# Kernel optimization log

Hardware: AMD Instinct MI355X
Metric: run time of the kernel (lower is better)

The kernel has to match this reference:

```python
import jax, jax.numpy as jnp
import numpy as np

INPUT_DIM, HIDDEN, CB_DIM, CB_SIZE = 768, 512, 256, 512
COMMIT_W = 1.0


def setup_inputs() -> dict:
    key = jax.random.key(0)
    ks = jax.random.split(key, 10)
    def lin(k, fan_in, fan_out):
        lim = 1.0 / np.sqrt(fan_in)
        return jax.random.uniform(k, (fan_in, fan_out), jnp.float32, -lim, lim)
    return {
        "x": jax.random.normal(ks[0], (32, 2048, INPUT_DIM), jnp.float32),
        "W1": lin(ks[1], INPUT_DIM, HIDDEN),
        "b1": jnp.zeros((HIDDEN,), jnp.float32),
        "W2": lin(ks[2], HIDDEN, CB_DIM),
        "b2": jnp.zeros((CB_DIM,), jnp.float32),
        "codebook": jax.random.normal(ks[3], (CB_SIZE, CB_DIM), jnp.float32),
        "W3": lin(ks[4], CB_DIM, HIDDEN),
        "b3": jnp.zeros((HIDDEN,), jnp.float32),
        "W4": lin(ks[5], HIDDEN, INPUT_DIM),
        "b4": jnp.zeros((INPUT_DIM,), jnp.float32),
    }


def reference(x, W1, b1, W2, b2, codebook, W3, b3, W4, b4):
    # encoder MLP: [b, n, 768] -> [b, n, 256]
    h = jax.nn.relu(jnp.einsum('bnd,dh->bnh', x, W1) + b1)
    z = jnp.einsum('bnh,hc->bnc', h, W2) + b2

    # VQ: squared-L2 distance to codebook, argmin, gather
    # d(z, c) = ||z||^2 - 2 z.c + ||c||^2  (||z||^2 constant over argmin, omitted)
    dots = jnp.einsum('bnc,kc->bnk', z, codebook)          # [b, n, K]
    c_sq = jnp.sum(codebook * codebook, axis=-1)            # [K]
    indices = jnp.argmin(c_sq - 2.0 * dots, axis=-1)        # [b, n] int
    q = codebook[indices]                                   # [b, n, 256] gather

    # straight-through estimator + commitment loss
    quantized = z + jax.lax.stop_gradient(q - z)
    commit_loss = COMMIT_W * jnp.mean((z - jax.lax.stop_gradient(q)) ** 2)

    # decoder MLP: [b, n, 256] -> [b, n, 768]
    h2 = jax.nn.relu(jnp.einsum('bnc,ch->bnh', quantized, W3) + b3)
    recon = jnp.einsum('bnh,hd->bnd', h2, W4) + b4
    return recon, indices.astype(jnp.int32), commit_loss
```

## Files before the change

### kernel.cpp

```cpp
#include <hip/hip_runtime.h>

typedef unsigned short u16;
typedef unsigned int   u32;
typedef __attribute__((ext_vector_type(8))) short short8;
typedef __attribute__((ext_vector_type(4))) float f32x4;

#define NTOK 65536
#define IND  768
#define HID  512
#define CBD  256
#define CBS  512

#define OUT_IDX_OFF   ((size_t)NTOK * IND)
#define OUT_LOSS_OFF  (OUT_IDX_OFF + NTOK)

#define OFF_H      ((size_t)0)
#define OFF_Z      ((size_t)134217728)
#define OFF_W1H    ((size_t)201326592)
#define OFF_W1L    ((size_t)202113024)
#define OFF_W2H    ((size_t)202899456)
#define OFF_W2L    ((size_t)203161600)
#define OFF_CBH    ((size_t)203423744)
#define OFF_CBL    ((size_t)203685888)
#define OFF_CSQ    ((size_t)203948032)
#define OFF_PART   ((size_t)0)
#define OFF_TABLE  ((size_t)8388608)
#define OFF_ZSQ    ((size_t)9961472)
#define OFF_IDX    ((size_t)10223616)
#define OFF_FLAGS  ((size_t)10485760)
#define OFF_CNT    ((size_t)10747904)

__device__ __forceinline__ u16 f2bf(float f) {
    u32 u = __float_as_uint(f);
    return (u16)((u + 0x7fffu + ((u >> 16) & 1u)) >> 16);
}
__device__ __forceinline__ float bf2f(u16 h) {
    return __uint_as_float(((u32)h) << 16);
}

__global__ __launch_bounds__(256) void cbsplit(
    const float* __restrict__ cb, u16* __restrict__ hi, u16* __restrict__ lo,
    float* __restrict__ csq)
{
    int c = blockIdx.x, t = threadIdx.x;
    float v = cb[(size_t)c * CBD + t];
    u16 h = f2bf(v); u16 l = f2bf(v - bf2f(h));
    hi[(size_t)c * CBD + t] = h; lo[(size_t)c * CBD + t] = l;
    __shared__ float red[256];
    red[t] = v * v; __syncthreads();
    for (int s = 128; s; s >>= 1) { if (t < s) red[t] += red[t + s]; __syncthreads(); }
    if (!t) csq[c] = red[0];
}

__global__ __launch_bounds__(256) void wsplit(
    const float* __restrict__ W, u16* __restrict__ hi, u16* __restrict__ lo,
    int K, int N)
{
    int n = blockIdx.x;
    for (int k = threadIdx.x; k < K; k += 256) {
        float v = W[(size_t)k * N + n];
        u16 h = f2bf(v); u16 l = f2bf(v - bf2f(h));
        hi[(size_t)n * K + k] = h; lo[(size_t)n * K + k] = l;
    }
}

#define CHS 1040
#define PLN (4 * CHS)

template<int AMODE, int EPI>
__global__ __launch_bounds__(256, 2) void gemm3(
    const float* __restrict__ Af, const u32* __restrict__ Apk,
    const u16* __restrict__ Bhi, const u16* __restrict__ Blo,
    const float* __restrict__ bias,
    u32* __restrict__ Opk, float* __restrict__ Opart,
    int M, int N, int K)
{
    __shared__ u16 lds[4 * PLN];
    u16* sAh = lds;
    u16* sAl = lds + PLN;
    u16* sBh = lds + 2 * PLN;
    u16* sBl = lds + 3 * PLN;
    const int tid  = threadIdx.x;

    const int nwg = gridDim.x * gridDim.y;
    const int hw  = blockIdx.y * gridDim.x + blockIdx.x;
    const int logical = (hw & 7) * (nwg >> 3) + (hw >> 3);
    const int bx = logical % gridDim.x;
    const int by = logical / gridDim.x;

    const int m0 = by * 128, n0 = bx * 128;
    const int w = tid >> 6, lane = tid & 63, quad = lane >> 4, l15 = lane & 15;
    const int wm = (w & 1) * 64, wn = (w >> 1) * 64;

    f32x4 acc[4][4] = {};

    for (int k0 = 0; k0 < K; k0 += 32) {
        __syncthreads();
        if (AMODE == 0) {
            #pragma unroll
            for (int s = 0; s < 4; ++s) {
                int slot = tid + s * 256;
                int m = slot >> 3, kg = (slot & 7) << 2;
                int c = kg >> 3, off = kg & 7;
                float4 v = *(const float4*)(Af + (size_t)(m0 + m) * K + k0 + kg);
                u16 h0 = f2bf(v.x), h1 = f2bf(v.y), h2 = f2bf(v.z), h3 = f2bf(v.w);
                ushort4 hv = {h0, h1, h2, h3};
                ushort4 lv = {f2bf(v.x - bf2f(h0)), f2bf(v.y - bf2f(h1)),
                              f2bf(v.z - bf2f(h2)), f2bf(v.w - bf2f(h3))};
                *(ushort4*)&sAh[c * CHS + m * 8 + off] = hv;
                *(ushort4*)&sAl[c * CHS + m * 8 + off] = lv;
            }
        } else {
            #pragma unroll
            for (int s = 0; s < 4; ++s) {
                int slot = tid + s * 256;
                int m = slot >> 3, ke = (slot & 7) << 2;
                int c = ke >> 3, off = ke & 7;
                uint4 u = *(const uint4*)(Apk + (size_t)(m0 + m) * K + k0 + ke);
                ushort4 hv = {(u16)(u.x & 0xffff), (u16)(u.y & 0xffff),
                              (u16)(u.z & 0xffff), (u16)(u.w & 0xffff)};
                ushort4 lv = {(u16)(u.x >> 16), (u16)(u.y >> 16),
                              (u16)(u.z >> 16), (u16)(u.w >> 16)};
                *(ushort4*)&sAh[c * CHS + m * 8 + off] = hv;
                *(ushort4*)&sAl[c * CHS + m * 8 + off] = lv;
            }
        }
        #pragma unroll
        for (int s = 0; s < 4; ++s) {
            int slot = tid + s * 256;
            int n = (slot & 511) >> 2, ku = slot & 3;
            const u16* src = (slot < 512) ? Bhi : Blo;
            u16* dst = (slot < 512) ? sBh : sBl;
            uint4 u = *(const uint4*)(src + (size_t)(n0 + n) * K + k0 + ku * 8);
            *(uint4*)&dst[ku * CHS + n * 8] = u;
        }
        __syncthreads();

        short8 ah[4], al[4], bh[4], bl[4];
        const int kc = quad * CHS;
        #pragma unroll
        for (int i = 0; i < 4; ++i) {
            int ar = wm + i * 16 + l15;
            int br = wn + i * 16 + l15;
            ah[i] = *(const short8*)&sAh[kc + ar * 8];
            al[i] = *(const short8*)&sAl[kc + ar * 8];
            bh[i] = *(const short8*)&sBh[kc + br * 8];
            bl[i] = *(const short8*)&sBl[kc + br * 8];
        }
        #pragma unroll
        for (int i = 0; i < 4; ++i)
            #pragma unroll
            for (int j = 0; j < 4; ++j) {
                acc[i][j] = __builtin_amdgcn_mfma_f32_16x16x32_bf16(ah[i], bh[j], acc[i][j], 0, 0, 0);
                acc[i][j] = __builtin_amdgcn_mfma_f32_16x16x32_bf16(ah[i], bl[j], acc[i][j], 0, 0, 0);
                acc[i][j] = __builtin_amdgcn_mfma_f32_16x16x32_bf16(al[i], bh[j], acc[i][j], 0, 0, 0);
            }
    }

    if (EPI <= 1) {
        float bn[4];
        #pragma unroll
        for (int j = 0; j < 4; ++j) bn[j] = bias[n0 + wn + j * 16 + l15];
        #pragma unroll
        for (int i = 0; i < 4; ++i)
            #pragma unroll
            for (int r = 0; r < 4; ++r) {
                int row = m0 + wm + i * 16 + quad * 4 + r;
                #pragma unroll
                for (int j = 0; j < 4; ++j) {
                    float v = acc[i][j][r] + bn[j];
                    if (EPI == 0) v = fmaxf(v, 0.f);
                    u16 h = f2bf(v); u16 l = f2bf(v - bf2f(h));
                    Opk[(size_t)row * N + n0 + wn + j * 16 + l15] = (u32)h | ((u32)l << 16);
                }
            }
    } else {
        float cs[4]; int cidx[4];
        #pragma unroll
        for (int j = 0; j < 4; ++j) {
            cidx[j] = n0 + wn + j * 16 + l15;
            cs[j] = bias[cidx[j]];
        }
        const int nparts = gridDim.x * 2;
        const int pslot  = bx * 2 + (w >> 1);
        #pragma unroll
        for (int i = 0; i < 4; ++i)
            #pragma unroll
            for (int r = 0; r < 4; ++r) {
                int row = m0 + wm + i * 16 + quad * 4 + r;
                float d1 = 3.4e38f, d2 = 3.4e38f; int i1 = 0x7fffffff;
                #pragma unroll
                for (int j = 0; j < 4; ++j) {
                    float v = fmaf(-2.0f, acc[i][j][r], cs[j]);
                    if (v < d1) { d2 = d1; d1 = v; i1 = cidx[j]; }
                    else d2 = fminf(d2, v);
                }
                #pragma unroll
                for (int mm = 1; mm < 16; mm <<= 1) {
                    float od1 = __shfl_xor(d1, mm, 64);
                    float od2 = __shfl_xor(d2, mm, 64);
                    int   oi1 = __shfl_xor(i1, mm, 64);
                    if (od1 < d1 || (od1 == d1 && oi1 < i1)) { d2 = fminf(d1, od2); d1 = od1; i1 = oi1; }
                    else d2 = fminf(d2, od1);
                }
                if (l15 == 0) {
                    float4 o = {d1, d2, __int_as_float(i1), 0.f};
                    *(float4*)&Opart[((size_t)row * nparts + pslot) * 4] = o;
                }
            }
    }
}

__global__ __launch_bounds__(256) void zsq_pk(
    const u32* __restrict__ Zpk, float* __restrict__ zsq)
{
    int tok = blockIdx.x * 4 + (threadIdx.x >> 6);
    int lane = threadIdx.x & 63;
    uint4 u = *(const uint4*)(Zpk + (size_t)tok * CBD + lane * 4);
    float z0 = bf2f((u16)(u.x & 0xffff)) + bf2f((u16)(u.x >> 16));
    float z1 = bf2f((u16)(u.y & 0xffff)) + bf2f((u16)(u.y >> 16));
    float z2 = bf2f((u16)(u.z & 0xffff)) + bf2f((u16)(u.z >> 16));
    float z3 = bf2f((u16)(u.w & 0xffff)) + bf2f((u16)(u.w >> 16));
    float s = z0 * z0 + z1 * z1 + z2 * z2 + z3 * z3;
    #pragma unroll
    for (int off = 32; off; off >>= 1) s += __shfl_down(s, off, 64);
    if (!lane) zsq[tok] = s;
}

__global__ __launch_bounds__(256) void vq_reduce(
    const float* __restrict__ part, const float* __restrict__ zsq,
    float* __restrict__ out_idx, int* __restrict__ idx_i,
    int* __restrict__ cnt, float* __restrict__ accum, int* __restrict__ flags)
{
    int tok = blockIdx.x * 256 + threadIdx.x;
    float d1 = 3.4e38f, d2 = 3.4e38f; int i1 = 0x7fffffff;
    #pragma unroll
    for (int nb = 0; nb < 8; ++nb) {
        float4 p = *(const float4*)&part[((size_t)tok * 8 + nb) * 4];
        float pd1 = p.x, pd2 = p.y; int pi1 = __float_as_int(p.z);
        if (pd1 < d1 || (pd1 == d1 && pi1 < i1)) { d2 = fminf(d1, pd2); d1 = pd1; i1 = pi1; }
        else d2 = fminf(d2, pd1);
    }
    out_idx[tok] = (float)i1;
    idx_i[tok] = i1;
    if (d2 - d1 < 0.01f) {
        int p = atomicAdd(cnt, 1);
        if (p >= 0 && p < NTOK) flags[p] = tok;
    }
    float c = zsq[tok] + d1;
    __shared__ float red[256];
    red[threadIdx.x] = c; __syncthreads();
    for (int s = 128; s; s >>= 1) { if (threadIdx.x < s) red[threadIdx.x] += red[threadIdx.x + s]; __syncthreads(); }
    if (!threadIdx.x) atomicAdd(accum, red[0]);
}

__device__ __forceinline__ void fma16(float (&a)[4][4],
    float x0, float x1, float x2, float x3, float4 w)
{
    a[0][0] = fmaf(x0, w.x, a[0][0]); a[0][1] = fmaf(x0, w.y, a[0][1]);
    a[0][2] = fmaf(x0, w.z, a[0][2]); a[0][3] = fmaf(x0, w.w, a[0][3]);
    a[1][0] = fmaf(x1, w.x, a[1][0]); a[1][1] = fmaf(x1, w.y, a[1][1]);
    a[1][2] = fmaf(x1, w.z, a[1][2]); a[1][3] = fmaf(x1, w.w, a[1][3]);
    a[2][0] = fmaf(x2, w.x, a[2][0]); a[2][1] = fmaf(x2, w.y, a[2][1]);
    a[2][2] = fmaf(x2, w.z, a[2][2]); a[2][3] = fmaf(x2, w.w, a[2][3]);
    a[3][0] = fmaf(x3, w.x, a[3][0]); a[3][1] = fmaf(x3, w.y, a[3][1]);
    a[3][2] = fmaf(x3, w.z, a[3][2]); a[3][3] = fmaf(x3, w.w, a[3][3]);
}
__device__ __forceinline__ void fma8(float (&a)[2][4],
    float x0, float x1, float4 w)
{
    a[0][0] = fmaf(x0, w.x, a[0][0]); a[0][1] = fmaf(x0, w.y, a[0][1]);
    a[0][2] = fmaf(x0, w.z, a[0][2]); a[0][3] = fmaf(x0, w.w, a[0][3]);
    a[1][0] = fmaf(x1, w.x, a[1][0]); a[1][1] = fmaf(x1, w.y, a[1][1]);
    a[1][2] = fmaf(x1, w.z, a[1][2]); a[1][3] = fmaf(x1, w.w, a[1][3]);
}

__global__ __launch_bounds__(256) void fixup(
    const int* __restrict__ cnt, const int* __restrict__ flags,
    const float* __restrict__ x, const float* __restrict__ W1, const float* __restrict__ b1,
    const float* __restrict__ W2, const float* __restrict__ b2,
    const float* __restrict__ cb, const float* __restrict__ csq,
    int* __restrict__ idx_i, float* __restrict__ out_idx)
{
    __shared__ float xs[8][IND];
    __shared__ float hs[8][HID];
    __shared__ float zs[8][CBD];
    __shared__ float csq_s[CBS];
    __shared__ float bd_s[4][8];
    __shared__ int   bi_s[4][8];
    __shared__ int   tok_s[8];

    int n = cnt[0]; if (n > NTOK) n = NTOK; if (n < 0) n = 0;
    const int t = threadIdx.x;
    const int nb = (n + 7) >> 3;

    if (t < 128) *(float4*)&csq_s[t * 4] = *(const float4*)(csq + t * 4);

    for (int ib = blockIdx.x; ib < nb; ib += gridDim.x) {
        const int base = ib * 8;
        __syncthreads();
        if (t < 8) {
            int fi = base + t; if (fi > n - 1) fi = n - 1;
            tok_s[t] = flags[fi];
        }
        __syncthreads();

        #pragma unroll
        for (int s = 0; s < 6; ++s) {
            int slot = t + s * 256;
            int tt = slot / 192, c4 = slot - tt * 192;
            *(float4*)&xs[tt][c4 * 4] =
                *(const float4*)(x + (size_t)tok_s[tt] * IND + c4 * 4);
        }
        __syncthreads();

        {
            const int tg4 = (t >> 7) * 4;
            const int j0 = (t & 127) * 4;
            float a[4][4];
            float4 bb = *(const float4*)(b1 + j0);
            #pragma unroll
            for (int ti = 0; ti < 4; ++ti) {
                a[ti][0] = bb.x; a[ti][1] = bb.y; a[ti][2] = bb.z; a[ti][3] = bb.w;
            }
            const float* Wb = W1 + j0;
#define LW1(s, K4) { const int _k = (((K4) < 192) ? (K4) : 191) * 2048;        \
            s##0 = *(const float4*)(Wb + _k);                                  \
            s##1 = *(const float4*)(Wb + _k + 512);                            \
            s##2 = *(const float4*)(Wb + _k + 1024);                           \
            s##3 = *(const float4*)(Wb + _k + 1536); }
#define CMP1(s, K4) {                                                          \
            float4 xv0 = *(const float4*)&xs[tg4 + 0][(K4) * 4];               \
            float4 xv1 = *(const float4*)&xs[tg4 + 1][(K4) * 4];               \
            float4 xv2 = *(const float4*)&xs[tg4 + 2][(K4) * 4];               \
            float4 xv3 = *(const float4*)&xs[tg4 + 3][(K4) * 4];               \
            fma16(a, xv0.x, xv1.x, xv2.x, xv3.x, s##0);                        \
            fma16(a, xv0.y, xv1.y, xv2.y, xv3.y, s##1);                        \
            fma16(a, xv0.z, xv1.z, xv2.z, xv3.z, s##2);                        \
            fma16(a, xv0.w, xv1.w, xv2.w, xv3.w, s##3); }
            float4 wA0, wA1, wA2, wA3, wB0, wB1, wB2, wB3;
            float4 wC0, wC1, wC2, wC3, wD0, wD1, wD2, wD3;
            LW1(wA, 0); LW1(wB, 1); LW1(wC, 2);
            for (int k4 = 0; k4 < 192; k4 += 4) {
                LW1(wD, k4 + 3); CMP1(wA, k4 + 0);
                LW1(wA, k4 + 4); CMP1(wB, k4 + 1);
                LW1(wB, k4 + 5); CMP1(wC, k4 + 2);
                LW1(wC, k4 + 6); CMP1(wD, k4 + 3);
            }
#undef LW1
#undef CMP1
            #pragma unroll
            for (int ti = 0; ti < 4; ++ti) {
                float4 o = {fmaxf(a[ti][0], 0.f), fmaxf(a[ti][1], 0.f),
                            fmaxf(a[ti][2], 0.f), fmaxf(a[ti][3], 0.f)};
                *(float4*)&hs[tg4 + ti][j0] = o;
            }
        }
        __syncthreads();

        {
            const int tg2 = (t >> 6) * 2;
            const int c0 = (t & 63) * 4;
            float az[2][4];
            float4 bz = *(const float4*)(b2 + c0);
            #pragma unroll
            for (int ti = 0; ti < 2; ++ti) {
                az[ti][0] = bz.x; az[ti][1] = bz.y; az[ti][2] = bz.z; az[ti][3] = bz.w;
            }
            const float* Wb = W2 + c0;
#define LW2(s, K4) { const int _k = (((K4) < 128) ? (K4) : 127) * 1024;        \
            s##0 = *(const float4*)(Wb + _k);                                  \
            s##1 = *(const float4*)(Wb + _k + 256);                            \
            s##2 = *(const float4*)(Wb + _k + 512);                            \
            s##3 = *(const float4*)(Wb + _k + 768); }
#define CMP2(s, K4) {                                                          \
            float4 hv0 = *(const float4*)&hs[tg2 + 0][(K4) * 4];               \
            float4 hv1 = *(const float4*)&hs[tg2 + 1][(K4) * 4];               \
            fma8(az, hv0.x, hv1.x, s##0);                                      \
            fma8(az, hv0.y, hv1.y, s##1);                                      \
            fma8(az, hv0.z, hv1.z, s##2);                                      \
            fma8(az, hv0.w, hv1.w, s##3); }
            float4 wA0, wA1, wA2, wA3, wB0, wB1, wB2, wB3;
            float4 wC0, wC1, wC2, wC3, wD0, wD1, wD2, wD3;
            LW2(wA, 0); LW2(wB, 1); LW2(wC, 2);
            for (int k4 = 0; k4 < 128; k4 += 4) {
                LW2(wD, k4 + 3); CMP2(wA, k4 + 0);
                LW2(wA, k4 + 4); CMP2(wB, k4 + 1);
                LW2(wB, k4 + 5); CMP2(wC, k4 + 2);
                LW2(wC, k4 + 6); CMP2(wD, k4 + 3);
            }
#undef LW2
#undef CMP2
            #pragma unroll
            for (int ti = 0; ti < 2; ++ti) {
                float4 o = {az[ti][0], az[ti][1], az[ti][2], az[ti][3]};
                *(float4*)&zs[tg2 + ti][c0] = o;
            }
        }
        __syncthreads();

        {
            const int wv = t >> 6, l = t & 63;
            const float* cb0 = cb + (size_t)t * CBD;
            const float* cb1 = cb + (size_t)(t + 256) * CBD;
            float d0[8], d1[8];
            #pragma unroll
            for (int tt = 0; tt < 8; ++tt) { d0[tt] = 0.f; d1[tt] = 0.f; }
            float4 pA = *(const float4*)(cb0);
            float4 pB = *(const float4*)(cb1);
            for (int k4 = 0; k4 < 64; ++k4) {
                float4 cA = pA, cB = pB;
                int kn = (k4 + 1 < 64) ? (k4 + 1) : 63;
                pA = *(const float4*)(cb0 + kn * 4);
                pB = *(const float4*)(cb1 + kn * 4);
                #pragma unroll
                for (int tt = 0; tt < 8; ++tt) {
                    float4 zv = *(const float4*)&zs[tt][k4 * 4];
                    d0[tt] = fmaf(zv.w, cA.w, fmaf(zv.z, cA.z,
                             fmaf(zv.y, cA.y, fmaf(zv.x, cA.x, d0[tt]))));
                    d1[tt] = fmaf(zv.w, cB.w, fmaf(zv.z, cB.z,
                             fmaf(zv.y, cB.y, fmaf(zv.x, cB.x, d1[tt]))));
                }
            }
            float bd[8]; int bi[8];
            const float cs0 = csq_s[t], cs1 = csq_s[t + 256];
            #pragma unroll
            for (int tt = 0; tt < 8; ++tt) {
                float e0 = cs0 - 2.f * d0[tt];
                float e1 = cs1 - 2.f * d1[tt];
                if (e0 <= e1) { bd[tt] = e0; bi[tt] = t; }
                else          { bd[tt] = e1; bi[tt] = t + 256; }
            }
            #pragma unroll
            for (int mm = 1; mm < 64; mm <<= 1) {
                #pragma unroll
                for (int tt = 0; tt < 8; ++tt) {
                    float od = __shfl_xor(bd[tt], mm, 64);
                    int   oi = __shfl_xor(bi[tt], mm, 64);
                    if (od < bd[tt] || (od == bd[tt] && oi < bi[tt])) { bd[tt] = od; bi[tt] = oi; }
                }
            }
            if (l == 0) {
                #pragma unroll
                for (int tt = 0; tt < 8; ++tt) { bd_s[wv][tt] = bd[tt]; bi_s[wv][tt] = bi[tt]; }
            }
        }
        __syncthreads();

        if (t < 8) {
            const int tt = t;
            float d = bd_s[0][tt]; int i = bi_s[0][tt];
            #pragma unroll
            for (int wv = 1; wv < 4; ++wv) {
                float od = bd_s[wv][tt]; int oi = bi_s[wv][tt];
                if (od < d || (od == d && oi < i)) { d = od; i = oi; }
            }
            if (base + tt < n) {
                int tok = tok_s[tt];
                idx_i[tok] = i; out_idx[tok] = (float)i;
            }
        }
        __syncthreads();
    }
}

__global__ __launch_bounds__(256) void table_pre(
    const float* __restrict__ cb, const float* __restrict__ W3,
    const float* __restrict__ b3, const float* __restrict__ W4,
    const float* __restrict__ b4, float* __restrict__ table)
{
    __shared__ float crow[CBD];
    __shared__ float h2[HID];
    const int c = blockIdx.x;
    const int t = threadIdx.x;
    crow[t] = cb[(size_t)c * CBD + t];
    __syncthreads();
    #pragma unroll
    for (int s = 0; s < 2; ++s) {
        int j = t + s * 256;
        float acc = b3[j];
        for (int k = 0; k < CBD; ++k) acc = fmaf(crow[k], W3[(size_t)k * HID + j], acc);
        h2[j] = fmaxf(acc, 0.f);
    }
    __syncthreads();
    #pragma unroll
    for (int s = 0; s < 3; ++s) {
        int j = t + s * 256;
        float acc = b4[j];
        for (int k = 0; k < HID; ++k) acc = fmaf(h2[k], W4[(size_t)k * IND + j], acc);
        table[(size_t)c * IND + j] = acc;
    }
}

__global__ __launch_bounds__(256) void gather_kernel(
    const int* __restrict__ idx, const float* __restrict__ table,
    float* __restrict__ out)
{
    unsigned i = blockIdx.x * 256u + threadIdx.x;
    unsigned tok = i / 192u;
    unsigned c = i - tok * 192u;
    int id = idx[tok];
    ((float4*)out)[i] = ((const float4*)table)[(size_t)id * 192 + c];
}

__global__ void finalize_kernel(const float* __restrict__ accum,
                                float* __restrict__ out_loss)
{
    out_loss[0] = accum[0] * (1.0f / 16777216.0f);
}

extern "C" void kernel_launch(void* const* d_in, const int* in_sizes, int n_in,
                              void* d_out, int out_size, void* d_ws, size_t ws_size,
                              hipStream_t stream) {
    const float* x  = (const float*)d_in[0];
    const float* W1 = (const float*)d_in[1];
    const float* b1 = (const float*)d_in[2];
    const float* W2 = (const float*)d_in[3];
    const float* b2 = (const float*)d_in[4];
    const float* cb = (const float*)d_in[5];
    const float* W3 = (const float*)d_in[6];
    const float* b3 = (const float*)d_in[7];
    const float* W4 = (const float*)d_in[8];
    const float* b4 = (const float*)d_in[9];

    char* ws = (char*)d_ws;
    u32*  Hpk   = (u32*)(ws + OFF_H);
    u32*  Zpk   = (u32*)(ws + OFF_Z);
    u16*  W1h   = (u16*)(ws + OFF_W1H);
    u16*  W1l   = (u16*)(ws + OFF_W1L);
    u16*  W2h   = (u16*)(ws + OFF_W2H);
    u16*  W2l   = (u16*)(ws + OFF_W2L);
    u16*  CBh   = (u16*)(ws + OFF_CBH);
    u16*  CBl   = (u16*)(ws + OFF_CBL);
    float* csq  = (float*)(ws + OFF_CSQ);
    float* part = (float*)(ws + OFF_PART);
    float* table = (float*)(ws + OFF_TABLE);
    float* zsq  = (float*)(ws + OFF_ZSQ);
    int*   idx_i = (int*)(ws + OFF_IDX);
    int*   flags = (int*)(ws + OFF_FLAGS);
    int*   cnt   = (int*)(ws + OFF_CNT);
    float* accum = (float*)(ws + OFF_CNT + 4);

    float* out      = (float*)d_out;
    float* out_idx  = out + OUT_IDX_OFF;
    float* out_loss = out + OUT_LOSS_OFF;

    cbsplit<<<CBS, 256, 0, stream>>>(cb, CBh, CBl, csq);
    wsplit<<<HID, 256, 0, stream>>>(W1, W1h, W1l, IND, HID);
    wsplit<<<CBD, 256, 0, stream>>>(W2, W2h, W2l, HID, CBD);

    gemm3<0, 0><<<dim3(HID / 128, NTOK / 128), 256, 0, stream>>>(
        x, (const u32*)nullptr, W1h, W1l, b1, Hpk, (float*)nullptr, NTOK, HID, IND);
    gemm3<1, 1><<<dim3(CBD / 128, NTOK / 128), 256, 0, stream>>>(
        (const float*)nullptr, Hpk, W2h, W2l, b2, Zpk, (float*)nullptr, NTOK, CBD, HID);

    hipMemsetAsync(cnt, 0, 8, stream);

    zsq_pk<<<NTOK / 4, 256, 0, stream>>>(Zpk, zsq);

    gemm3<1, 2><<<dim3(CBS / 128, NTOK / 128), 256, 0, stream>>>(
        (const float*)nullptr, Zpk, CBh, CBl, csq, (u32*)nullptr, part, NTOK, CBS, CBD);

    table_pre<<<CBS, 256, 0, stream>>>(cb, W3, b3, W4, b4, table);

    vq_reduce<<<NTOK / 256, 256, 0, stream>>>(part, zsq, out_idx, idx_i, cnt, accum, flags);

    fixup<<<1024, 256, 0, stream>>>(cnt, flags, x, W1, b1, W2, b2, cb, csq, idx_i, out_idx);

    gather_kernel<<<(NTOK * (IND / 4)) / 256, 256, 0, stream>>>(idx_i, table, out);

    finalize_kernel<<<1, 1, 0, stream>>>(accum, out_loss);
}
```

Before: 972.9 us.

## Split fp32 VQ fixup into tiled batched GEMM passes over flagged tokens

The single fused fixup kernel, which recomputed encoder and distances for 8 flagged tokens at a time while streaming W1/W2 from global memory, is replaced by three kernels. Two are a 64x64 shared-memory tiled fp32 GEMM, the first gathering flagged rows of x and the second producing z, followed by a distance/argmin kernel that processes 32 tokens per block. Work is done in chunks of up to 32768 flagged tokens, with intermediates staged in workspace. This gives weight reuse across many tokens, at the cost of six extra launches and intermediate global traffic even when few tokens are flagged.

Measured after the change: 875.6 us. 10.0% less time.

```diff
diff --git a/kernel.cpp b/kernel.cpp
--- a/kernel.cpp
+++ b/kernel.cpp
@@ -29,6 +29,9 @@
 #define OFF_IDX    ((size_t)10223616)
 #define OFF_FLAGS  ((size_t)10485760)
 #define OFF_CNT    ((size_t)10747904)
+#define OFF_HFIX   ((size_t)16777216)
+#define OFF_ZFIX   ((size_t)83886080)
+#define FCHUNK 32768
 
 __device__ __forceinline__ u16 f2bf(float f) {
     u32 u = __float_as_uint(f);
@@ -266,141 +269,120 @@
     a[3][0] = fmaf(x3, w.x, a[3][0]); a[3][1] = fmaf(x3, w.y, a[3][1]);
     a[3][2] = fmaf(x3, w.z, a[3][2]); a[3][3] = fmaf(x3, w.w, a[3][3]);
 }
-__device__ __forceinline__ void fma8(float (&a)[2][4],
-    float x0, float x1, float4 w)
-{
-    a[0][0] = fmaf(x0, w.x, a[0][0]); a[0][1] = fmaf(x0, w.y, a[0][1]);
-    a[0][2] = fmaf(x0, w.z, a[0][2]); a[0][3] = fmaf(x0, w.w, a[0][3]);
-    a[1][0] = fmaf(x1, w.x, a[1][0]); a[1][1] = fmaf(x1, w.y, a[1][1]);
-    a[1][2] = fmaf(x1, w.z, a[1][2]); a[1][3] = fmaf(x1, w.w, a[1][3]);
-}
-
-__global__ __launch_bounds__(256) void fixup(
-    const int* __restrict__ cnt, const int* __restrict__ flags,
-    const float* __restrict__ x, const float* __restrict__ W1, const float* __restrict__ b1,
-    const float* __restrict__ W2, const float* __restrict__ b2,
-    const float* __restrict__ cb, const float* __restrict__ csq,
+
+template<int K, int N, int RELU, int MODE>
+__global__ __launch_bounds__(256) void fixup_gemm(
+    const int* __restrict__ cnt, const int* __restrict__ flags, int base,
+    const float* __restrict__ A, const float* __restrict__ W,
+    const float* __restrict__ bias, float* __restrict__ C)
+{
+    __shared__ float xs[64][68];
+    __shared__ float Wt[64][68];
+    __shared__ int   tok_s[64];
+    int n = cnt[0]; if (n > NTOK) n = NTOK;
+    int nc = n - base; if (nc <= 0) return; if (nc > FCHUNK) nc = FCHUNK;
+    const int ntile = (nc + 63) >> 6;
+    const int items = ntile * (N >> 6);
+    const int t = threadIdx.x;
+    const int tg4 = (t >> 4) << 2;
+    const int cg  = t & 15;
+
+    for (int it = blockIdx.x; it < items; it += gridDim.x) {
+        const int tt = it / (N >> 6);
+        const int ct = it - tt * (N >> 6);
+        const int j0 = ct * 64;
+        const int trow = tt * 64;
+        __syncthreads();
+        if (MODE == 0 && t < 64) {
+            int fi = base + trow + t; if (fi > n - 1) fi = n - 1;
+            tok_s[t] = flags[fi];
+        }
+        __syncthreads();
+
+        float a[4][4];
+        float4 bb = *(const float4*)(bias + j0 + cg * 4);
+        #pragma unroll
+        for (int ti = 0; ti < 4; ++ti) {
+            a[ti][0] = bb.x; a[ti][1] = bb.y; a[ti][2] = bb.z; a[ti][3] = bb.w;
+        }
+
+        for (int k0 = 0; k0 < K; k0 += 64) {
+            __syncthreads();
+            #pragma unroll
+            for (int s = 0; s < 4; ++s) {
+                int slot = t + s * 256;
+                int row = slot >> 4, c4 = slot & 15;
+                const float* src = (MODE == 0)
+                    ? A + (size_t)tok_s[row] * K + k0 + c4 * 4
+                    : A + (size_t)(trow + row) * K + k0 + c4 * 4;
+                *(float4*)&xs[row][c4 * 4] = *(const float4*)src;
+            }
+            #pragma unroll
+            for (int s = 0; s < 4; ++s) {
+                int slot = t + s * 256;
+                int kk = slot >> 4, c4 = slot & 15;
+                *(float4*)&Wt[kk][c4 * 4] =
+                    *(const float4*)(W + (size_t)(k0 + kk) * N + j0 + c4 * 4);
+            }
+            __syncthreads();
+            #pragma unroll 4
+            for (int k4 = 0; k4 < 16; ++k4) {
+                float4 xv0 = *(const float4*)&xs[tg4 + 0][k4 * 4];
+                float4 xv1 = *(const float4*)&xs[tg4 + 1][k4 * 4];
+                float4 xv2 = *(const float4*)&xs[tg4 + 2][k4 * 4];
+                float4 xv3 = *(const float4*)&xs[tg4 + 3][k4 * 4];
+                float4 w0 = *(const float4*)&Wt[k4 * 4 + 0][cg * 4];
+                float4 w1 = *(const float4*)&Wt[k4 * 4 + 1][cg * 4];
+                float4 w2 = *(const float4*)&Wt[k4 * 4 + 2][cg * 4];
+                float4 w3 = *(const float4*)&Wt[k4 * 4 + 3][cg * 4];
+                fma16(a, xv0.x, xv1.x, xv2.x, xv3.x, w0);
+                fma16(a, xv0.y, xv1.y, xv2.y, xv3.y, w1);
+                fma16(a, xv0.z, xv1.z, xv2.z, xv3.z, w2);
+                fma16(a, xv0.w, xv1.w, xv2.w, xv3.w, w3);
+            }
+        }
+        #pragma unroll
+        for (int ti = 0; ti < 4; ++ti) {
+            float4 o;
+            if (RELU) {
+                o.x = fmaxf(a[ti][0], 0.f); o.y = fmaxf(a[ti][1], 0.f);
+                o.z = fmaxf(a[ti][2], 0.f); o.w = fmaxf(a[ti][3], 0.f);
+            } else {
+                o.x = a[ti][0]; o.y = a[ti][1]; o.z = a[ti][2]; o.w = a[ti][3];
+            }
+            *(float4*)&C[(size_t)(trow + tg4 + ti) * N + j0 + cg * 4] = o;
+        }
+    }
+}
+
+__global__ __launch_bounds__(256) void fixup_d(
+    const int* __restrict__ cnt, const int* __restrict__ flags, int base,
+    const float* __restrict__ zbuf, const float* __restrict__ cb,
+    const float* __restrict__ csq,
     int* __restrict__ idx_i, float* __restrict__ out_idx)
 {
-    __shared__ float xs[8][IND];
-    __shared__ float hs[8][HID];
-    __shared__ float zs[8][CBD];
+    __shared__ float zs[32][CBD];
     __shared__ float csq_s[CBS];
     __shared__ float bd_s[4][8];
     __shared__ int   bi_s[4][8];
-    __shared__ int   tok_s[8];
-
-    int n = cnt[0]; if (n > NTOK) n = NTOK; if (n < 0) n = 0;
+    int n = cnt[0]; if (n > NTOK) n = NTOK;
+    int nc = n - base; if (nc <= 0) return; if (nc > FCHUNK) nc = FCHUNK;
+    const int ntile = (nc + 31) >> 5;
     const int t = threadIdx.x;
-    const int nb = (n + 7) >> 3;
-
+    const int wv = t >> 6, l = t & 63;
     if (t < 128) *(float4*)&csq_s[t * 4] = *(const float4*)(csq + t * 4);
 
-    for (int ib = blockIdx.x; ib < nb; ib += gridDim.x) {
-        const int base = ib * 8;
+    for (int it = blockIdx.x; it < ntile; it += gridDim.x) {
         __syncthreads();
-        if (t < 8) {
-            int fi = base + t; if (fi > n - 1) fi = n - 1;
-            tok_s[t] = flags[fi];
+        #pragma unroll
+        for (int s = 0; s < 8; ++s) {
+            int slot = t + s * 256;
+            int row = slot >> 6, c4 = slot & 63;
+            *(float4*)&zs[row][c4 * 4] =
+                *(const float4*)(zbuf + (size_t)(it * 32 + row) * CBD + c4 * 4);
         }
         __syncthreads();
-
-        #pragma unroll
-        for (int s = 0; s < 6; ++s) {
-            int slot = t + s * 256;
-            int tt = slot / 192, c4 = slot - tt * 192;
-            *(float4*)&xs[tt][c4 * 4] =
-                *(const float4*)(x + (size_t)tok_s[tt] * IND + c4 * 4);
-        }
-        __syncthreads();
-
-        {
-            const int tg4 = (t >> 7) * 4;
-            const int j0 = (t & 127) * 4;
-            float a[4][4];
-            float4 bb = *(const float4*)(b1 + j0);
-            #pragma unroll
-            for (int ti = 0; ti < 4; ++ti) {
-                a[ti][0] = bb.x; a[ti][1] = bb.y; a[ti][2] = bb.z; a[ti][3] = bb.w;
-            }
-            const float* Wb = W1 + j0;
-#define LW1(s, K4) { const int _k = (((K4) < 192) ? (K4) : 191) * 2048;        \
-            s##0 = *(const float4*)(Wb + _k);                                  \
-            s##1 = *(const float4*)(Wb + _k + 512);                            \
-            s##2 = *(const float4*)(Wb + _k + 1024);                           \
-            s##3 = *(const float4*)(Wb + _k + 1536); }
-#define CMP1(s, K4) {                                                          \
-            float4 xv0 = *(const float4*)&xs[tg4 + 0][(K4) * 4];               \
-            float4 xv1 = *(const float4*)&xs[tg4 + 1][(K4) * 4];               \
-            float4 xv2 = *(const float4*)&xs[tg4 + 2][(K4) * 4];               \
-            float4 xv3 = *(const float4*)&xs[tg4 + 3][(K4) * 4];               \
-            fma16(a, xv0.x, xv1.x, xv2.x, xv3.x, s##0);                        \
-            fma16(a, xv0.y, xv1.y, xv2.y, xv3.y, s##1);                        \
-            fma16(a, xv0.z, xv1.z, xv2.z, xv3.z, s##2);                        \
-            fma16(a, xv0.w, xv1.w, xv2.w, xv3.w, s##3); }
-            float4 wA0, wA1, wA2, wA3, wB0, wB1, wB2, wB3;
-            float4 wC0, wC1, wC2, wC3, wD0, wD1, wD2, wD3;
-            LW1(wA, 0); LW1(wB, 1); LW1(wC, 2);
-            for (int k4 = 0; k4 < 192; k4 += 4) {
-                LW1(wD, k4 + 3); CMP1(wA, k4 + 0);
-                LW1(wA, k4 + 4); CMP1(wB, k4 + 1);
-                LW1(wB, k4 + 5); CMP1(wC, k4 + 2);
-                LW1(wC, k4 + 6); CMP1(wD, k4 + 3);
-            }
-#undef LW1
-#undef CMP1
-            #pragma unroll
-            for (int ti = 0; ti < 4; ++ti) {
-                float4 o = {fmaxf(a[ti][0], 0.f), fmaxf(a[ti][1], 0.f),
-                            fmaxf(a[ti][2], 0.f), fmaxf(a[ti][3], 0.f)};
-                *(float4*)&hs[tg4 + ti][j0] = o;
-            }
-        }
-        __syncthreads();
-
-        {
-            const int tg2 = (t >> 6) * 2;
-            const int c0 = (t & 63) * 4;
-            float az[2][4];
-            float4 bz = *(const float4*)(b2 + c0);
-            #pragma unroll
-            for (int ti = 0; ti < 2; ++ti) {
-                az[ti][0] = bz.x; az[ti][1] = bz.y; az[ti][2] = bz.z; az[ti][3] = bz.w;
-            }
-            const float* Wb = W2 + c0;
-#define LW2(s, K4) { const int _k = (((K4) < 128) ? (K4) : 127) * 1024;        \
-            s##0 = *(const float4*)(Wb + _k);                                  \
-            s##1 = *(const float4*)(Wb + _k + 256);                            \
-            s##2 = *(const float4*)(Wb + _k + 512);                            \
-            s##3 = *(const float4*)(Wb + _k + 768); }
-#define CMP2(s, K4) {                                                          \
-            float4 hv0 = *(const float4*)&hs[tg2 + 0][(K4) * 4];               \
-            float4 hv1 = *(const float4*)&hs[tg2 + 1][(K4) * 4];               \
-            fma8(az, hv0.x, hv1.x, s##0);                                      \
-            fma8(az, hv0.y, hv1.y, s##1);                                      \
-            fma8(az, hv0.z, hv1.z, s##2);                                      \
-            fma8(az, hv0.w, hv1.w, s##3); }
-            float4 wA0, wA1, wA2, wA3, wB0, wB1, wB2, wB3;
-            float4 wC0, wC1, wC2, wC3, wD0, wD1, wD2, wD3;
-            LW2(wA, 0); LW2(wB, 1); LW2(wC, 2);
-            for (int k4 = 0; k4 < 128; k4 += 4) {
-                LW2(wD, k4 + 3); CMP2(wA, k4 + 0);
-                LW2(wA, k4 + 4); CMP2(wB, k4 + 1);
-                LW2(wB, k4 + 5); CMP2(wC, k4 + 2);
-                LW2(wC, k4 + 6); CMP2(wD, k4 + 3);
-            }
-#undef LW2
-#undef CMP2
-            #pragma unroll
-            for (int ti = 0; ti < 2; ++ti) {
-                float4 o = {az[ti][0], az[ti][1], az[ti][2], az[ti][3]};
-                *(float4*)&zs[tg2 + ti][c0] = o;
-            }
-        }
-        __syncthreads();
-
-        {
-            const int wv = t >> 6, l = t & 63;
+        for (int sb = 0; sb < 4; ++sb) {
             const float* cb0 = cb + (size_t)t * CBD;
             const float* cb1 = cb + (size_t)(t + 256) * CBD;
             float d0[8], d1[8];
@@ -415,7 +397,7 @@
                 pB = *(const float4*)(cb1 + kn * 4);
                 #pragma unroll
                 for (int tt = 0; tt < 8; ++tt) {
-                    float4 zv = *(const float4*)&zs[tt][k4 * 4];
+                    float4 zv = *(const float4*)&zs[sb * 8 + tt][k4 * 4];
                     d0[tt] = fmaf(zv.w, cA.w, fmaf(zv.z, cA.z,
                              fmaf(zv.y, cA.y, fmaf(zv.x, cA.x, d0[tt]))));
                     d1[tt] = fmaf(zv.w, cB.w, fmaf(zv.z, cB.z,
@@ -444,23 +426,23 @@
                 #pragma unroll
                 for (int tt = 0; tt < 8; ++tt) { bd_s[wv][tt] = bd[tt]; bi_s[wv][tt] = bi[tt]; }
             }
-        }
-        __syncthreads();
-
-        if (t < 8) {
-            const int tt = t;
-            float d = bd_s[0][tt]; int i = bi_s[0][tt];
-            #pragma unroll
-            for (int wv = 1; wv < 4; ++wv) {
-                float od = bd_s[wv][tt]; int oi = bi_s[wv][tt];
-                if (od < d || (od == d && oi < i)) { d = od; i = oi; }
-            }
-            if (base + tt < n) {
-                int tok = tok_s[tt];
-                idx_i[tok] = i; out_idx[tok] = (float)i;
-            }
-        }
-        __syncthreads();
+            __syncthreads();
+            if (t < 8) {
+                const int tt = t;
+                float d = bd_s[0][tt]; int i = bi_s[0][tt];
+                #pragma unroll
+                for (int v2 = 1; v2 < 4; ++v2) {
+                    float od = bd_s[v2][tt]; int oi = bi_s[v2][tt];
+                    if (od < d || (od == d && oi < i)) { d = od; i = oi; }
+                }
+                int fi = base + it * 32 + sb * 8 + tt;
+                if (fi < n) {
+                    int tok = flags[fi];
+                    idx_i[tok] = i; out_idx[tok] = (float)i;
+                }
+            }
+            __syncthreads();
+        }
     }
 }
 
@@ -540,6 +522,8 @@
     int*   flags = (int*)(ws + OFF_FLAGS);
     int*   cnt   = (int*)(ws + OFF_CNT);
     float* accum = (float*)(ws + OFF_CNT + 4);
+    float* hfix  = (float*)(ws + OFF_HFIX);
+    float* zfix  = (float*)(ws + OFF_ZFIX);
 
     float* out      = (float*)d_out;
     float* out_idx  = out + OUT_IDX_OFF;
@@ -565,7 +549,15 @@
 
     vq_reduce<<<NTOK / 256, 256, 0, stream>>>(part, zsq, out_idx, idx_i, cnt, accum, flags);
 
-    fixup<<<1024, 256, 0, stream>>>(cnt, flags, x, W1, b1, W2, b2, cb, csq, idx_i, out_idx);
+    for (int pass = 0; pass < 2; ++pass) {
+        int base = pass * FCHUNK;
+        fixup_gemm<IND, HID, 1, 0><<<1024, 256, 0, stream>>>(
+            cnt, flags, base, x, W1, b1, hfix);
+        fixup_gemm<HID, CBD, 0, 1><<<512, 256, 0, stream>>>(
+            cnt, flags, base, hfix, W2, b2, zfix);
+        fixup_d<<<512, 256, 0, stream>>>(
+            cnt, flags, base, zfix, cb, csq, idx_i, out_idx);
+    }
 
     gather_kernel<<<(NTOK * (IND / 4)) / 256, 256, 0, stream>>>(idx_i, table, out);
 
```
